# Optimization experiments

Hardware: AMD Instinct MI355X
Metric: run time of the kernel (lower is better)

## Reference

```python
import jax, jax.numpy as jnp
import numpy as np

N, E, K = 50000, 800000, 16
D, H = 128, 8
DH = D // H
SCALE = D ** (-0.5)
EPS = 1e-5


def _ln(x, g, b):
    m = jnp.mean(x, axis=-1, keepdims=True)
    v = jnp.mean((x - m) ** 2, axis=-1, keepdims=True)
    return (x - m) * jax.lax.rsqrt(v + EPS) * g + b


def setup_inputs() -> dict:
    key = jax.random.key(0)
    ks = jax.random.split(key, 20)
    s = 0.02
    inp = {
        "triplet_h": jax.random.normal(ks[0], (N, D), jnp.float32),
        "mask_nodes": jnp.ones((N,), jnp.bool_),
        "src": jax.random.randint(ks[1], (E,), 0, N),
        "dst": jax.random.randint(ks[2], (E,), 0, N),
        "edge_bias": jax.random.normal(ks[3], (E, H), jnp.float32),
        "mask_edges": jnp.ones((E,), jnp.bool_),
        "inc_idx": jax.random.randint(ks[4], (N, K), 0, E),
        "inc_mask": jnp.ones((N, K), jnp.bool_),
        # params
        "ln1_g": jnp.ones((D,), jnp.float32),
        "ln1_b": jnp.zeros((D,), jnp.float32),
        "qkv_w": jax.random.normal(ks[5], (D, 3 * D), jnp.float32) * s,
        "qkv_b": jnp.zeros((3 * D,), jnp.float32),
        "res_in_w": jax.random.normal(ks[6], (D, D), jnp.float32) * s,
        "res_in_b": jnp.zeros((D,), jnp.float32),
        "res_ln_g": jnp.ones((D,), jnp.float32),
        "res_ln_b": jnp.zeros((D,), jnp.float32),
        "ffn_in_w": jax.random.normal(ks[7], (D, 4 * D), jnp.float32) * s,
        "ffn_in_b": jnp.zeros((4 * D,), jnp.float32),
        "ffn_out_w": jax.random.normal(ks[8], (4 * D, D), jnp.float32) * s,
        "ffn_out_b": jnp.zeros((D,), jnp.float32),
    }
    return inp


def reference(triplet_h, mask_nodes, src, dst, edge_bias, mask_edges, inc_idx,
              inc_mask, ln1_g, ln1_b, qkv_w, qkv_b, res_in_w, res_in_b,
              res_ln_g, res_ln_b, ffn_in_w, ffn_in_b, ffn_out_w, ffn_out_b):
    x = _ln(triplet_h, ln1_g, ln1_b)
    qkv = (x @ qkv_w + qkv_b).reshape(-1, 3, H, DH)
    q = qkv[:, 0] * SCALE  # [N,H,dh]
    k = qkv[:, 1]
    v = qkv[:, 2]

    zero_i = jnp.zeros_like(src)
    se = jnp.where(mask_edges, src, zero_i)
    de = jnp.where(mask_edges, dst, zero_i)

    dot_all = jnp.sum(q[se] * k[de], axis=-1)  # [E,H]
    me = mask_edges[:, None]
    dot_all = jnp.where(me, dot_all, 0.0)
    eb = jnp.where(me, edge_bias, 0.0)
    scores_all = dot_all + eb  # [E,H]

    v_src = jnp.where(me[:, :, None], v[se], 0.0)  # [E,H,dh]

    idx = jnp.clip(inc_idx, 0)  # [N,K]
    s_in = scores_all[idx]  # [N,K,H]
    v_in = v_src[idx]       # [N,K,H,dh]
    m_in = inc_mask & mask_nodes[:, None]
    s_in = jnp.where(m_in[:, :, None], s_in, -1e9)
    a_in = jax.nn.softmax(s_in, axis=1)  # [N,K,H]
    out = jnp.sum(v_in * a_in[..., None], axis=1).reshape(-1, H * DH)  # [N,D]

    # Residual block (dropout p=0)
    x2 = triplet_h + (out @ res_in_w + res_in_b)
    y = _ln(x2, res_ln_g, res_ln_b)
    y = jax.nn.gelu(y @ ffn_in_w + ffn_in_b) @ ffn_out_w + ffn_out_b
    return x2 + y
```

## Files before the change

### kernel.cpp

```cpp
#include <hip/hip_runtime.h>
#include <math.h>

#define N_NODES 50000
#define N_EDGES 800000
#define QSCALE 0.08838834764831845f
#define LEPS 1e-5f

typedef unsigned short ushort_t;
typedef unsigned char uchar_t;
typedef short bf16x8 __attribute__((ext_vector_type(8)));
typedef float f32x4 __attribute__((ext_vector_type(4)));
typedef float f32x2 __attribute__((ext_vector_type(2)));

__device__ __forceinline__ ushort_t f2b(float f) {
    unsigned int u = __float_as_uint(f);
    u += 0x7FFF + ((u >> 16) & 1);
    return (ushort_t)(u >> 16);
}
__device__ __forceinline__ uchar_t f2fp8(float f) {
    unsigned int pk = __builtin_amdgcn_cvt_pk_fp8_f32(f, f, 0, false);
    return (uchar_t)(pk & 0xff);
}
__device__ __forceinline__ float gelu_f(float x) {
    float u = 1.5957691216057308f * (x + 0.044715f * x * x * x);
    float e = __expf(u);
    float t = 1.f - 2.f / (e + 1.f);
    return 0.5f * x * (1.f + t);
}
__device__ __forceinline__ void gload16(const ushort_t* g, ushort_t* l) {
    __builtin_amdgcn_global_load_lds(
        (const __attribute__((address_space(1))) unsigned int*)g,
        (__attribute__((address_space(3))) unsigned int*)l, 16, 0, 0);
}
__device__ __forceinline__ int frag_idx(int n7, int k7) {
    return ((n7 >> 4) * 4 + (k7 >> 5)) * 512 + ((k7 >> 3) & 3) * 128 + (n7 & 15) * 8 + (k7 & 7);
}
__device__ __forceinline__ int fidx64(int n7, int k6) {
    return ((n7 >> 4) * 2 + (k6 >> 5)) * 512 + ((k6 >> 3) & 3) * 128 + (n7 & 15) * 8 + (k6 & 7);
}

__global__ __launch_bounds__(256) void k_prep(
    const float* __restrict__ qkvw, const float* __restrict__ riw,
    const float* __restrict__ fiw,  const float* __restrict__ fow,
    ushort_t* __restrict__ qkvwT, ushort_t* __restrict__ riwT,
    ushort_t* __restrict__ fiwT,  ushort_t* __restrict__ fowT)
{
    int i = blockIdx.x * 256 + threadIdx.x;
    if (i < 384 * 128) {
        int n = i >> 7, k = i & 127;
        int ch = n >> 7, n7 = n & 127, half = k >> 6, k6 = k & 63;
        qkvwT[(size_t)(ch * 2 + half) * 8192 + fidx64(n7, k6)] = f2b(qkvw[k * 384 + n]);
        return;
    }
    i -= 384 * 128;
    if (i < 128 * 128) {
        int n = i >> 7, k = i & 127;
        riwT[frag_idx(n, k)] = f2b(riw[k * 128 + n]);
        return;
    }
    i -= 128 * 128;
    if (i < 512 * 128) {
        int n = i >> 7, k = i & 127;
        fiwT[(size_t)(n >> 7) * 16384 + frag_idx(n & 127, k)] = f2b(fiw[k * 512 + n]);
        return;
    }
    i -= 512 * 128;
    if (i < 128 * 512) {
        int n = i >> 9, k = i & 511;
        fowT[(size_t)(k >> 7) * 16384 + frag_idx(n, k & 127)] = f2b(fow[k * 128 + n]);
    }
}

__global__ __launch_bounds__(256) void k1_ln_qkv(
    const float* __restrict__ th, const float* __restrict__ g1, const float* __restrict__ b1,
    const ushort_t* __restrict__ wT, const float* __restrict__ bias,
    uchar_t* __restrict__ q8, uchar_t* __restrict__ k8, uchar_t* __restrict__ v8)
{
    __shared__ __align__(16) ushort_t xs[64][136];
    __shared__ __align__(16) ushort_t wbuf[8192];
    const int tid = threadIdx.x, lane = tid & 63, w = tid >> 6;
    const int g0 = blockIdx.x * 64;
    const bf16x8* wb8 = (const bf16x8*)wbuf;
    uchar_t* sbuf8 = (uchar_t*)xs;

    float ga = g1[lane], gb = g1[lane + 64];
    float ba = b1[lane], bb = b1[lane + 64];
    for (int rr = 0; rr < 16; ++rr) {
        int r = w * 16 + rr, grow = g0 + r;
        float x0 = 0.f, x1 = 0.f;
        if (grow < N_NODES) {
            x0 = th[(size_t)grow * 128 + lane];
            x1 = th[(size_t)grow * 128 + 64 + lane];
        }
        float s1 = x0 + x1, s2 = x0 * x0 + x1 * x1;
        #pragma unroll
        for (int off = 32; off; off >>= 1) { s1 += __shfl_xor(s1, off); s2 += __shfl_xor(s2, off); }
        float m = s1 * (1.f / 128.f);
        float v = s2 * (1.f / 128.f) - m * m;
        float rs = rsqrtf(v + LEPS);
        xs[r][lane]      = f2b((x0 - m) * rs * ga + ba);
        xs[r][lane + 64] = f2b((x1 - m) * rs * gb + bb);
    }
    __syncthreads();

    const int q = lane >> 4, ml = lane & 15;
    const int rloc = w * 16 + q * 4;
    bf16x8 a[4];
    #pragma unroll
    for (int kc = 0; kc < 4; ++kc)
        a[kc] = *(const bf16x8*)&xs[w * 16 + ml][kc * 32 + q * 8];

    for (int ch = 0; ch < 3; ++ch) {
        f32x4 acc[8];
        #pragma unroll
        for (int t2 = 0; t2 < 8; ++t2) acc[t2] = (f32x4){0.f, 0.f, 0.f, 0.f};
        #pragma unroll
        for (int half = 0; half < 2; ++half) {
            __syncthreads();
            #pragma unroll
            for (int t = 0; t < 4; ++t)
                gload16(wT + (size_t)(ch * 2 + half) * 8192 + (t * 256 + tid) * 8,
                        wbuf + (t * 256 + tid) * 8);
            __syncthreads();
            #pragma unroll
            for (int t2 = 0; t2 < 8; ++t2)
                #pragma unroll
                for (int kc2 = 0; kc2 < 2; ++kc2)
                    acc[t2] = __builtin_amdgcn_mfma_f32_16x16x32_bf16(
                        a[half * 2 + kc2], wb8[(t2 * 2 + kc2) * 64 + lane], acc[t2], 0, 0, 0);
        }
        #pragma unroll
        for (int t2 = 0; t2 < 8; ++t2) {
            int n = t2 * 16 + ml;
            float bs = bias[ch * 128 + n];
            #pragma unroll
            for (int r = 0; r < 4; ++r)
                sbuf8[(rloc + r) * 128 + n] = f2fp8(acc[t2][r] + bs);
        }
        __syncthreads();
        uchar_t* outp = (ch == 0) ? q8 : (ch == 1) ? k8 : v8;
        int grow = g0 + (tid >> 2);
        if (grow < N_NODES) {
            uint4 v0 = *(const uint4*)(sbuf8 + tid * 32);
            uint4 v1 = *(const uint4*)(sbuf8 + tid * 32 + 16);
            *(uint4*)(outp + (size_t)grow * 128 + (tid & 3) * 32) = v0;
            *(uint4*)(outp + (size_t)grow * 128 + (tid & 3) * 32 + 16) = v1;
        }
    }
}

__global__ __launch_bounds__(256) void k23_agg(
    const uchar_t* __restrict__ q8, const uchar_t* __restrict__ k8,
    const uchar_t* __restrict__ v8,
    const int* __restrict__ src, const int* __restrict__ dst,
    const int* __restrict__ inc_idx, const float* __restrict__ eb,
    ushort_t* __restrict__ outw)
{
    __shared__ int es[32];
    __shared__ int ss[32];
    __shared__ int ds[32];
    __shared__ float sc[2][16][8];
    const int tid = threadIdx.x;
    const int nb = blockIdx.x * 2;

    if (tid < 32) {
        int n = nb + (tid >> 4);
        int e = inc_idx[(size_t)n * 16 + (tid & 15)];
        if (e < 0) e = 0;
        es[tid] = e;
        ss[tid] = src[e];
        ds[tid] = dst[e];
    }
    __syncthreads();
    {
        int pair = tid >> 3, h = tid & 7;
        int e = es[pair], s = ss[pair], d = ds[pair];
        uint4 qa = *(const uint4*)(q8 + (size_t)s * 128 + h * 16);
        uint4 ka = *(const uint4*)(k8 + (size_t)d * 128 + h * 16);
        const unsigned int* qu = (const unsigned int*)&qa;
        const unsigned int* ku = (const unsigned int*)&ka;
        float acc = 0.f;
        #pragma unroll
        for (int j = 0; j < 4; ++j) {
            f32x2 q0 = __builtin_amdgcn_cvt_pk_f32_fp8(qu[j], false);
            f32x2 q1 = __builtin_amdgcn_cvt_pk_f32_fp8(qu[j], true);
            f32x2 k0 = __builtin_amdgcn_cvt_pk_f32_fp8(ku[j], false);
            f32x2 k1 = __builtin_amdgcn_cvt_pk_f32_fp8(ku[j], true);
            acc = fmaf(q0.x, k0.x, acc); acc = fmaf(q0.y, k0.y, acc);
            acc = fmaf(q1.x, k1.x, acc); acc = fmaf(q1.y, k1.y, acc);
        }
        sc[pair >> 4][pair & 15][h] = acc * QSCALE + eb[(size_t)e * 8 + h];
    }
    __syncthreads();

    const int loc = tid >> 7;
    const int j = tid & 127;
    const int h = j >> 4;
    float m = -1e30f;
    #pragma unroll
    for (int k = 0; k < 16; k++) m = fmaxf(m, sc[loc][k][h]);
    float p[16];
    float sum = 0.f;
    #pragma unroll
    for (int k = 0; k < 16; k++) { p[k] = __expf(sc[loc][k][h] - m); sum += p[k]; }
    float inv = 1.f / sum;
    float acc = 0.f;
    #pragma unroll
    for (int k = 0; k < 16; k++)
        acc += p[k] * __builtin_amdgcn_cvt_f32_fp8((int)v8[(size_t)ss[loc * 16 + k] * 128 + j], 0);
    outw[(size_t)(nb + loc) * 128 + j] = f2b(acc * inv);
}

__global__ __launch_bounds__(256) void k4_ffn(
    const float* __restrict__ th, const ushort_t* __restrict__ outw,
    const ushort_t* __restrict__ riwT, const float* __restrict__ rib,
    const float* __restrict__ rlg, const float* __restrict__ rlb,
    const ushort_t* __restrict__ fiwT, const float* __restrict__ fib,
    const ushort_t* __restrict__ fowT, const float* __restrict__ fob,
    float* __restrict__ dout)
{
    __shared__ __align__(16) ushort_t sbuf[64][136];
    __shared__ __align__(16) ushort_t wbuf[16384];
    const int tid = threadIdx.x, lane = tid & 63, w = tid >> 6;
    const int g0 = blockIdx.x * 64;
    const int q = lane >> 4, ml = lane & 15;
    const int rloc = w * 16 + q * 4;
    const int aswz = (ml >> 2) & 3;
    const bf16x8* wb8 = (const bf16x8*)wbuf;

    #pragma unroll
    for (int t = 0; t < 8; ++t)
        gload16(riwT + (size_t)(t * 256 + tid) * 8, wbuf + (t * 256 + tid) * 8);

    int arow = g0 + w * 16 + ml; if (arow > N_NODES - 1) arow = N_NODES - 1;
    bf16x8 a[4];
    #pragma unroll
    for (int kc = 0; kc < 4; ++kc)
        a[kc] = *(const bf16x8*)(outw + (size_t)arow * 128 + kc * 32 + q * 8);
    __syncthreads();

    f32x4 x2[8];
    #pragma unroll
    for (int t = 0; t < 8; ++t) {
        f32x4 acc = {0.f, 0.f, 0.f, 0.f};
        #pragma unroll
        for (int kc = 0; kc < 4; ++kc)
            acc = __builtin_amdgcn_mfma_f32_16x16x32_bf16(
                a[kc], wb8[(t * 4 + kc) * 64 + lane], acc, 0, 0, 0);
        x2[t] = acc;
    }
    #pragma unroll
    for (int t = 0; t < 8; ++t) {
        float bb = rib[t * 16 + ml];
        #pragma unroll
        for (int r = 0; r < 4; ++r) {
            int grow = g0 + rloc + r;
            float tv = (grow < N_NODES) ? th[(size_t)grow * 128 + t * 16 + ml] : 0.f;
            x2[t][r] += bb + tv;
        }
    }

    {
        float rg[8], rbv[8];
        #pragma unroll
        for (int t = 0; t < 8; ++t) { rg[t] = rlg[t * 16 + ml]; rbv[t] = rlb[t * 16 + ml]; }
        #pragma unroll
        for (int r = 0; r < 4; ++r) {
            float s1 = 0.f, s2 = 0.f;
            #pragma unroll
            for (int t = 0; t < 8; ++t) { float v = x2[t][r]; s1 += v; s2 += v * v; }
            #pragma unroll
            for (int off = 1; off < 16; off <<= 1) { s1 += __shfl_xor(s1, off); s2 += __shfl_xor(s2, off); }
            float m = s1 * (1.f / 128.f);
            float v = s2 * (1.f / 128.f) - m * m;
            float rs = rsqrtf(v + LEPS);
            #pragma unroll
            for (int t = 0; t < 8; ++t) {
                int G = (2 * t + (ml >> 3)) ^ q;
                sbuf[rloc + r][G * 8 + (ml & 7)] = f2b((x2[t][r] - m) * rs * rg[t] + rbv[t]);
            }
        }
    }
    __syncthreads();

    bf16x8 a2[4];
    #pragma unroll
    for (int kc = 0; kc < 4; ++kc)
        a2[kc] = *(const bf16x8*)&sbuf[w * 16 + ml][(((kc * 4 + q) ^ aswz) << 3)];

    f32x4 y2[8];
    #pragma unroll
    for (int t = 0; t < 8; ++t) y2[t] = (f32x4){0.f, 0.f, 0.f, 0.f};

    for (int c4 = 0; c4 < 4; ++c4) {
        __syncthreads();
        #pragma unroll
        for (int t = 0; t < 8; ++t)
            gload16(fiwT + (size_t)c4 * 16384 + (t * 256 + tid) * 8, wbuf + (t * 256 + tid) * 8);
        __syncthreads();
        #pragma unroll
        for (int t2 = 0; t2 < 8; ++t2) {
            f32x4 hacc = {0.f, 0.f, 0.f, 0.f};
            #pragma unroll
            for (int kc = 0; kc < 4; ++kc)
                hacc = __builtin_amdgcn_mfma_f32_16x16x32_bf16(
                    a2[kc], wb8[(t2 * 4 + kc) * 64 + lane], hacc, 0, 0, 0);
            float fb = fib[c4 * 128 + t2 * 16 + ml];
            int G = (2 * t2 + (ml >> 3)) ^ q;
            #pragma unroll
            for (int r = 0; r < 4; ++r)
                sbuf[rloc + r][G * 8 + (ml & 7)] = f2b(gelu_f(hacc[r] + fb));
        }
        __syncthreads();
        #pragma unroll
        for (int t = 0; t < 8; ++t)
            gload16(fowT + (size_t)c4 * 16384 + (t * 256 + tid) * 8, wbuf + (t * 256 + tid) * 8);
        __syncthreads();
        bf16x8 a3[4];
        #pragma unroll
        for (int kc = 0; kc < 4; ++kc)
            a3[kc] = *(const bf16x8*)&sbuf[w * 16 + ml][(((kc * 4 + q) ^ aswz) << 3)];
        #pragma unroll
        for (int t = 0; t < 8; ++t) {
            #pragma unroll
            for (int kc = 0; kc < 4; ++kc)
                y2[t] = __builtin_amdgcn_mfma_f32_16x16x32_bf16(
                    a3[kc], wb8[(t * 4 + kc) * 64 + lane], y2[t], 0, 0, 0);
        }
    }

    #pragma unroll
    for (int t = 0; t < 8; ++t) {
        float ob = fob[t * 16 + ml];
        #pragma unroll
        for (int r = 0; r < 4; ++r) {
            int grow = g0 + rloc + r;
            if (grow < N_NODES)
                dout[(size_t)grow * 128 + t * 16 + ml] = x2[t][r] + y2[t][r] + ob;
        }
    }
}

extern "C" void kernel_launch(void* const* d_in, const int* in_sizes, int n_in,
                              void* d_out, int out_size, void* d_ws, size_t ws_size,
                              hipStream_t stream)
{
    const float* th    = (const float*)d_in[0];
    const int*   src   = (const int*)d_in[2];
    const int*   dst   = (const int*)d_in[3];
    const float* ebias = (const float*)d_in[4];
    const int*   inc   = (const int*)d_in[6];
    const float* ln1g  = (const float*)d_in[8];
    const float* ln1b  = (const float*)d_in[9];
    const float* qkvw  = (const float*)d_in[10];
    const float* qkvb  = (const float*)d_in[11];
    const float* riw   = (const float*)d_in[12];
    const float* rib   = (const float*)d_in[13];
    const float* rlg   = (const float*)d_in[14];
    const float* rlb   = (const float*)d_in[15];
    const float* fiw   = (const float*)d_in[16];
    const float* fib   = (const float*)d_in[17];
    const float* fow   = (const float*)d_in[18];
    const float* fob   = (const float*)d_in[19];

    char* ws = (char*)d_ws;
    uchar_t* q8      = (uchar_t*)ws;                               ws += (size_t)N_NODES * 128;
    uchar_t* k8      = (uchar_t*)ws;                               ws += (size_t)N_NODES * 128;
    uchar_t* v8      = (uchar_t*)ws;                               ws += (size_t)N_NODES * 128;
    ushort_t* outw   = (ushort_t*)ws;                              ws += (size_t)N_NODES * 128 * 2;
    ushort_t* qkvwT  = (ushort_t*)ws;                              ws += (size_t)384 * 128 * 2;
    ushort_t* riwT   = (ushort_t*)ws;                              ws += (size_t)128 * 128 * 2;
    ushort_t* fiwT   = (ushort_t*)ws;                              ws += (size_t)512 * 128 * 2;
    ushort_t* fowT   = (ushort_t*)ws;                              ws += (size_t)128 * 512 * 2;
    float* dout = (float*)d_out;

    k_prep<<<768, 256, 0, stream>>>(qkvw, riw, fiw, fow, qkvwT, riwT, fiwT, fowT);
    k1_ln_qkv<<<(N_NODES + 63) / 64, 256, 0, stream>>>(th, ln1g, ln1b, qkvwT, qkvb, q8, k8, v8);
    k23_agg<<<N_NODES / 2, 256, 0, stream>>>(q8, k8, v8, src, dst, inc, ebias, outw);
    k4_ffn<<<(N_NODES + 63) / 64, 256, 0, stream>>>(th, outw, riwT, rib, rlg, rlb,
                                                    fiwT, fib, fowT, fob, dout);
}
```

Baseline: 289.5 us.

## Process eight nodes per aggregation block, widen per-thread gathers, double FFN block size

```diff
diff --git a/kernel.cpp b/kernel.cpp
--- a/kernel.cpp
+++ b/kernel.cpp
@@ -37,6 +37,21 @@
 }
 __device__ __forceinline__ int fidx64(int n7, int k6) {
     return ((n7 >> 4) * 2 + (k6 >> 5)) * 512 + ((k6 >> 3) & 3) * 128 + (n7 & 15) * 8 + (k6 & 7);
+}
+__device__ __forceinline__ float dot16fp8(uint4 qa, uint4 ka) {
+    const unsigned int* qu = (const unsigned int*)&qa;
+    const unsigned int* ku = (const unsigned int*)&ka;
+    float acc = 0.f;
+    #pragma unroll
+    for (int j = 0; j < 4; ++j) {
+        f32x2 q0 = __builtin_amdgcn_cvt_pk_f32_fp8(qu[j], false);
+        f32x2 q1 = __builtin_amdgcn_cvt_pk_f32_fp8(qu[j], true);
+        f32x2 k0 = __builtin_amdgcn_cvt_pk_f32_fp8(ku[j], false);
+        f32x2 k1 = __builtin_amdgcn_cvt_pk_f32_fp8(ku[j], true);
+        acc = fmaf(q0.x, k0.x, acc); acc = fmaf(q0.y, k0.y, acc);
+        acc = fmaf(q1.x, k1.x, acc); acc = fmaf(q1.y, k1.y, acc);
+    }
+    return acc;
 }
 
 __global__ __launch_bounds__(256) void k_prep(
@@ -156,16 +171,15 @@
     const int* __restrict__ inc_idx, const float* __restrict__ eb,
     ushort_t* __restrict__ outw)
 {
-    __shared__ int es[32];
-    __shared__ int ss[32];
-    __shared__ int ds[32];
-    __shared__ float sc[2][16][8];
+    __shared__ int es[128];
+    __shared__ int ss[128];
+    __shared__ int ds[128];
+    __shared__ float sc[8][16][8];
     const int tid = threadIdx.x;
-    const int nb = blockIdx.x * 2;
-
-    if (tid < 32) {
-        int n = nb + (tid >> 4);
-        int e = inc_idx[(size_t)n * 16 + (tid & 15)];
+    const int nb = blockIdx.x * 8;
+
+    if (tid < 128) {
+        int e = inc_idx[(size_t)nb * 16 + tid];
         if (e < 0) e = 0;
         es[tid] = e;
         ss[tid] = src[e];
@@ -173,45 +187,49 @@
     }
     __syncthreads();
     {
-        int pair = tid >> 3, h = tid & 7;
+        int pair = tid >> 1, hb = (tid & 1) << 2;
         int e = es[pair], s = ss[pair], d = ds[pair];
-        uint4 qa = *(const uint4*)(q8 + (size_t)s * 128 + h * 16);
-        uint4 ka = *(const uint4*)(k8 + (size_t)d * 128 + h * 16);
-        const unsigned int* qu = (const unsigned int*)&qa;
-        const unsigned int* ku = (const unsigned int*)&ka;
-        float acc = 0.f;
-        #pragma unroll
-        for (int j = 0; j < 4; ++j) {
-            f32x2 q0 = __builtin_amdgcn_cvt_pk_f32_fp8(qu[j], false);
-            f32x2 q1 = __builtin_amdgcn_cvt_pk_f32_fp8(qu[j], true);
-            f32x2 k0 = __builtin_amdgcn_cvt_pk_f32_fp8(ku[j], false);
-            f32x2 k1 = __builtin_amdgcn_cvt_pk_f32_fp8(ku[j], true);
-            acc = fmaf(q0.x, k0.x, acc); acc = fmaf(q0.y, k0.y, acc);
-            acc = fmaf(q1.x, k1.x, acc); acc = fmaf(q1.y, k1.y, acc);
-        }
-        sc[pair >> 4][pair & 15][h] = acc * QSCALE + eb[(size_t)e * 8 + h];
+        const uint4* qp = (const uint4*)(q8 + (size_t)s * 128 + hb * 16);
+        const uint4* kp = (const uint4*)(k8 + (size_t)d * 128 + hb * 16);
+        uint4 qa0 = qp[0], qa1 = qp[1], qa2 = qp[2], qa3 = qp[3];
+        uint4 ka0 = kp[0], ka1 = kp[1], ka2 = kp[2], ka3 = kp[3];
+        float4 ebv = *(const float4*)(eb + (size_t)e * 8 + hb);
+        int node = pair >> 4, slot = pair & 15;
+        sc[node][slot][hb + 0] = dot16fp8(qa0, ka0) * QSCALE + ebv.x;
+        sc[node][slot][hb + 1] = dot16fp8(qa1, ka1) * QSCALE + ebv.y;
+        sc[node][slot][hb + 2] = dot16fp8(qa2, ka2) * QSCALE + ebv.z;
+        sc[node][slot][hb + 3] = dot16fp8(qa3, ka3) * QSCALE + ebv.w;
     }
     __syncthreads();
 
-    const int loc = tid >> 7;
-    const int j = tid & 127;
-    const int h = j >> 4;
+    const int node = tid >> 5;
+    const int j0 = (tid & 31) * 4;
+    const int h = j0 >> 4;
     float m = -1e30f;
     #pragma unroll
-    for (int k = 0; k < 16; k++) m = fmaxf(m, sc[loc][k][h]);
+    for (int k = 0; k < 16; k++) m = fmaxf(m, sc[node][k][h]);
     float p[16];
     float sum = 0.f;
     #pragma unroll
-    for (int k = 0; k < 16; k++) { p[k] = __expf(sc[loc][k][h] - m); sum += p[k]; }
+    for (int k = 0; k < 16; k++) { p[k] = __expf(sc[node][k][h] - m); sum += p[k]; }
     float inv = 1.f / sum;
-    float acc = 0.f;
-    #pragma unroll
-    for (int k = 0; k < 16; k++)
-        acc += p[k] * __builtin_amdgcn_cvt_f32_fp8((int)v8[(size_t)ss[loc * 16 + k] * 128 + j], 0);
-    outw[(size_t)(nb + loc) * 128 + j] = f2b(acc * inv);
-}
-
-__global__ __launch_bounds__(256) void k4_ffn(
+    float a0 = 0.f, a1 = 0.f, a2 = 0.f, a3 = 0.f;
+    #pragma unroll
+    for (int k = 0; k < 16; k++) {
+        unsigned int vv = *(const unsigned int*)(v8 + (size_t)ss[node * 16 + k] * 128 + j0);
+        f32x2 v0 = __builtin_amdgcn_cvt_pk_f32_fp8(vv, false);
+        f32x2 v1 = __builtin_amdgcn_cvt_pk_f32_fp8(vv, true);
+        float pk = p[k];
+        a0 = fmaf(pk, v0.x, a0); a1 = fmaf(pk, v0.y, a1);
+        a2 = fmaf(pk, v1.x, a2); a3 = fmaf(pk, v1.y, a3);
+    }
+    unsigned int lo = (unsigned int)f2b(a0 * inv) | ((unsigned int)f2b(a1 * inv) << 16);
+    unsigned int hi = (unsigned int)f2b(a2 * inv) | ((unsigned int)f2b(a3 * inv) << 16);
+    uint2 o; o.x = lo; o.y = hi;
+    *(uint2*)(outw + (size_t)(nb + node) * 128 + j0) = o;
+}
+
+__global__ __launch_bounds__(512) void k4_ffn(
     const float* __restrict__ th, const ushort_t* __restrict__ outw,
     const ushort_t* __restrict__ riwT, const float* __restrict__ rib,
     const float* __restrict__ rlg, const float* __restrict__ rlb,
@@ -219,18 +237,18 @@
     const ushort_t* __restrict__ fowT, const float* __restrict__ fob,
     float* __restrict__ dout)
 {
-    __shared__ __align__(16) ushort_t sbuf[64][136];
+    __shared__ __align__(16) ushort_t sbuf[128][136];
     __shared__ __align__(16) ushort_t wbuf[16384];
     const int tid = threadIdx.x, lane = tid & 63, w = tid >> 6;
-    const int g0 = blockIdx.x * 64;
+    const int g0 = blockIdx.x * 128;
     const int q = lane >> 4, ml = lane & 15;
     const int rloc = w * 16 + q * 4;
     const int aswz = (ml >> 2) & 3;
     const bf16x8* wb8 = (const bf16x8*)wbuf;
 
     #pragma unroll
-    for (int t = 0; t < 8; ++t)
-        gload16(riwT + (size_t)(t * 256 + tid) * 8, wbuf + (t * 256 + tid) * 8);
+    for (int t = 0; t < 4; ++t)
+        gload16(riwT + (size_t)(t * 512 + tid) * 8, wbuf + (t * 512 + tid) * 8);
 
     int arow = g0 + w * 16 + ml; if (arow > N_NODES - 1) arow = N_NODES - 1;
     bf16x8 a[4];
@@ -295,8 +313,8 @@
     for (int c4 = 0; c4 < 4; ++c4) {
         __syncthreads();
         #pragma unroll
-        for (int t = 0; t < 8; ++t)
-            gload16(fiwT + (size_t)c4 * 16384 + (t * 256 + tid) * 8, wbuf + (t * 256 + tid) * 8);
+        for (int t = 0; t < 4; ++t)
+            gload16(fiwT + (size_t)c4 * 16384 + (t * 512 + tid) * 8, wbuf + (t * 512 + tid) * 8);
         __syncthreads();
         #pragma unroll
         for (int t2 = 0; t2 < 8; ++t2) {
@@ -313,8 +331,8 @@
         }
         __syncthreads();
         #pragma unroll
-        for (int t = 0; t < 8; ++t)
-            gload16(fowT + (size_t)c4 * 16384 + (t * 256 + tid) * 8, wbuf + (t * 256 + tid) * 8);
+        for (int t = 0; t < 4; ++t)
+            gload16(fowT + (size_t)c4 * 16384 + (t * 512 + tid) * 8, wbuf + (t * 512 + tid) * 8);
         __syncthreads();
         bf16x8 a3[4];
         #pragma unroll
@@ -376,7 +394,7 @@
 
     k_prep<<<768, 256, 0, stream>>>(qkvw, riw, fiw, fow, qkvwT, riwT, fiwT, fowT);
     k1_ln_qkv<<<(N_NODES + 63) / 64, 256, 0, stream>>>(th, ln1g, ln1b, qkvwT, qkvb, q8, k8, v8);
-    k23_agg<<<N_NODES / 2, 256, 0, stream>>>(q8, k8, v8, src, dst, inc, ebias, outw);
-    k4_ffn<<<(N_NODES + 63) / 64, 256, 0, stream>>>(th, outw, riwT, rib, rlg, rlb,
-                                                    fiwT, fib, fowT, fob, dout);
-}
+    k23_agg<<<N_NODES / 8, 256, 0, stream>>>(q8, k8, v8, src, dst, inc, ebias, outw);
+    k4_ffn<<<(N_NODES + 127) / 128, 512, 0, stream>>>(th, outw, riwT, rib, rlg, rlb,
+                                                      fiwT, fib, fowT, fob, dout);
+}
```

Result: no change. 290.3 us (+0.3%).
